# Kernel optimization log

Measured on AMD Instinct MI355X. Metric: run time of the kernel, lower is better.

Reference implementation:

```python
import jax, jax.numpy as jnp
import numpy as np

N, E, IN_CH, C, H, L, NCLS = 4096, 131072, 512, 256, 4, 3, 2
DH = C // H  # MHA head dim


def _ln(x, g, b, eps=1e-5):
    mu = x.mean(-1, keepdims=True)
    var = ((x - mu) ** 2).mean(-1, keepdims=True)
    return (x - mu) * jax.lax.rsqrt(var + eps) * g + b


def _gelu(x):
    return jax.nn.gelu(x, approximate=False)  # torch nn.GELU default (erf)


def _gatv2(x, src, dst, wl, wr, att, b):
    # x: [N,C]; wl/wr: [H*C, C]; att: [H,C]; b: [C]
    xl = (x @ wl.T).reshape(N, H, C)  # source transform
    e = jax.nn.leaky_relu(xl[src] + (x @ wr.T).reshape(N, H, C)[dst], 0.2)  # [Et,H,C]
    score = jnp.einsum('ehc,hc->eh', e, att)  # [Et,H]
    m = jax.ops.segment_max(score, dst, num_segments=N)
    ex = jnp.exp(score - m[dst])
    denom = jax.ops.segment_sum(ex, dst, num_segments=N)
    alpha = ex / denom[dst]  # segment softmax over incoming edges
    out = jax.ops.segment_sum(alpha[:, :, None] * xl[src], dst, num_segments=N)
    return out.mean(axis=1) + b  # concat=False -> head mean


def _mha(x, in_w, in_b, out_w, out_b):
    qkv = x @ in_w.T + in_b  # [N,3C]
    q, k, v = [t.reshape(N, H, DH) for t in jnp.split(qkv, 3, axis=-1)]
    scores = jnp.einsum('nhd,mhd->hnm', q, k) / np.sqrt(DH)
    probs = jax.nn.softmax(scores, axis=-1)
    o = jnp.einsum('hnm,mhd->nhd', probs, v).reshape(N, C)
    return o @ out_w.T + out_b


def setup_inputs() -> dict:
    key = jax.random.key(0)
    ks = iter(jax.random.split(key, 64))
    s = lambda shape, sc=0.05: jax.random.normal(next(ks), shape, jnp.float32) * sc
    d = {
        'x': jax.random.normal(next(ks), (N, IN_CH), jnp.float32),
        'edge_index': jax.random.randint(next(ks), (2, E), 0, N, jnp.int32),
        'in_w': s((C, IN_CH)), 'in_b': jnp.zeros((C,), jnp.float32),
        'gat_wl': s((L, H * C, C)), 'gat_wr': s((L, H * C, C)),
        'gat_att': s((L, H, C)), 'gat_b': jnp.zeros((L, C), jnp.float32),
        'mha_in_w': s((L, 3 * C, C)), 'mha_in_b': jnp.zeros((L, 3 * C), jnp.float32),
        'mha_out_w': s((L, C, C)), 'mha_out_b': jnp.zeros((L, C), jnp.float32),
        'ln1_g': jnp.ones((L, C), jnp.float32), 'ln1_b': jnp.zeros((L, C), jnp.float32),
        'ln2_g': jnp.ones((L, C), jnp.float32), 'ln2_b': jnp.zeros((L, C), jnp.float32),
        'ln3_g': jnp.ones((L, C), jnp.float32), 'ln3_b': jnp.zeros((L, C), jnp.float32),
        'ffn_w1': s((L, 2 * C, C)), 'ffn_b1': jnp.zeros((L, 2 * C), jnp.float32),
        'ffn_w2': s((L, C, 2 * C)), 'ffn_b2': jnp.zeros((L, C), jnp.float32),
        'out_w1': s((C, C)), 'out_b1': jnp.zeros((C,), jnp.float32),
        'out_w2': s((NCLS, C)), 'out_b2': jnp.zeros((NCLS,), jnp.float32),
    }
    return d


def reference(x, edge_index, in_w, in_b, gat_wl, gat_wr, gat_att, gat_b,
              mha_in_w, mha_in_b, mha_out_w, mha_out_b,
              ln1_g, ln1_b, ln2_g, ln2_b, ln3_g, ln3_b,
              ffn_w1, ffn_b1, ffn_w2, ffn_b2,
              out_w1, out_b1, out_w2, out_b2):
    # add self loops (PyG GATv2Conv default)
    loop = jnp.arange(N, dtype=edge_index.dtype)
    src = jnp.concatenate([edge_index[0], loop])
    dst = jnp.concatenate([edge_index[1], loop])

    h = x @ in_w.T + in_b  # input_proj
    for l in range(L):
        local = _gatv2(h, src, dst, gat_wl[l], gat_wr[l], gat_att[l], gat_b[l])
        h = _ln(h + local, ln1_g[l], ln1_b[l])
        attn = _mha(h, mha_in_w[l], mha_in_b[l], mha_out_w[l], mha_out_b[l])
        h = _ln(h + attn, ln2_g[l], ln2_b[l])
        ffn = _gelu(h @ ffn_w1[l].T + ffn_b1[l]) @ ffn_w2[l].T + ffn_b2[l]
        h = _ln(h + ffn, ln3_g[l], ln3_b[l])
    h = _gelu(h @ out_w1.T + out_b1)
    return h @ out_w2.T + out_b2
```

## Files before the change

### kernel.cpp

```cpp
#include <hip/hip_runtime.h>
#include <cstdint>
#include <cstddef>

typedef unsigned short u16;
typedef __bf16 bf16x8 __attribute__((ext_vector_type(8)));
typedef float f32x4 __attribute__((ext_vector_type(4)));

constexpr int kN  = 4096;
constexpr int kE  = 131072;
constexpr int kET = kE + kN;
constexpr int kIn = 512;
constexpr int kC  = 256;
constexpr int kL  = 3;

constexpr int NSPLIT = 4;
constexpr int KSPAN  = kN / NSPLIT;
constexpr int NSTEP  = KSPAN / 64;

__device__ __forceinline__ u16 f2bf(float f) {
    unsigned u = __builtin_bit_cast(unsigned, f);
    u += 0x7fffu + ((u >> 16) & 1u);
    return (u16)(u >> 16);
}
__device__ __forceinline__ float bf2f(u16 s) {
    unsigned u = ((unsigned)s) << 16;
    return __builtin_bit_cast(float, u);
}
__device__ __forceinline__ float gelu_erf(float x) {
    return 0.5f * x * (1.f + erff(x * 0.70710678118654752f));
}
__device__ __forceinline__ void gload_lds16(const u16* gsrc, u16* ldst) {
    __builtin_amdgcn_global_load_lds(
        (const __attribute__((address_space(1))) unsigned int*)gsrc,
        (__attribute__((address_space(3))) unsigned int*)ldst, 16, 0, 0);
}
__device__ __forceinline__ float dpp_ror_add16(float x) {
    int t;
    t = __builtin_amdgcn_update_dpp(0, __builtin_bit_cast(int, x), 0x121, 0xf, 0xf, true);
    x += __builtin_bit_cast(float, t);
    t = __builtin_amdgcn_update_dpp(0, __builtin_bit_cast(int, x), 0x122, 0xf, 0xf, true);
    x += __builtin_bit_cast(float, t);
    t = __builtin_amdgcn_update_dpp(0, __builtin_bit_cast(int, x), 0x124, 0xf, 0xf, true);
    x += __builtin_bit_cast(float, t);
    t = __builtin_amdgcn_update_dpp(0, __builtin_bit_cast(int, x), 0x128, 0xf, 0xf, true);
    x += __builtin_bit_cast(float, t);
    return x;
}
__device__ __forceinline__ void unpack8(uint4 u, float* x) {
    x[0] = __builtin_bit_cast(float, u.x << 16);
    x[1] = __builtin_bit_cast(float, u.x & 0xffff0000u);
    x[2] = __builtin_bit_cast(float, u.y << 16);
    x[3] = __builtin_bit_cast(float, u.y & 0xffff0000u);
    x[4] = __builtin_bit_cast(float, u.z << 16);
    x[5] = __builtin_bit_cast(float, u.z & 0xffff0000u);
    x[6] = __builtin_bit_cast(float, u.w << 16);
    x[7] = __builtin_bit_cast(float, u.w & 0xffff0000u);
}

__global__ void cast_all(
    const float* __restrict__ x, const float* __restrict__ in_w,
    const float* __restrict__ gwl, const float* __restrict__ gwr,
    const float* __restrict__ minw, const float* __restrict__ moutw,
    const float* __restrict__ f1, const float* __restrict__ f2,
    const float* __restrict__ o1,
    u16* __restrict__ xbf, u16* __restrict__ wbf) {
    int i = blockIdx.x * 256 + threadIdx.x;
    if (i >= 1359872) return;
    const float* s;
    u16* dbase;
    int sj, dj;
    if (i < 524288) {
        s = x; dbase = xbf; sj = i; dj = i;
    } else if (i < 557056) {
        s = in_w; dbase = wbf; sj = i - 524288; dj = sj;
    } else if (i < 753664) {
        int j = i - 557056; int l = j >> 16, wi = j & 65535;
        s = gwl; dbase = wbf; sj = j; dj = 32768 + l * 131072 + wi;
    } else if (i < 950272) {
        int j = i - 753664; int l = j >> 16, wi = j & 65535;
        s = gwr; dbase = wbf; sj = j; dj = 32768 + l * 131072 + 65536 + wi;
    } else if (i < 1097728) {
        s = minw; dbase = wbf; sj = i - 950272; dj = 425984 + sj;
    } else if (i < 1146880) {
        s = moutw; dbase = wbf; sj = i - 1097728; dj = 573440 + sj;
    } else if (i < 1245184) {
        s = f1; dbase = wbf; sj = i - 1146880; dj = 622592 + sj;
    } else if (i < 1343488) {
        s = f2; dbase = wbf; sj = i - 1245184; dj = 720896 + sj;
    } else {
        s = o1; dbase = wbf; sj = i - 1343488; dj = 819200 + sj;
    }
    float4 v = ((const float4*)s)[sj];
    ushort4 o;
    o.x = f2bf(v.x); o.y = f2bf(v.y); o.z = f2bf(v.z); o.w = f2bf(v.w);
    ((ushort4*)dbase)[dj] = o;
}

__global__ void csr_count(const int* __restrict__ ei, int* __restrict__ cnt) {
    int e = blockIdx.x * 256 + threadIdx.x;
    if (e >= kET) return;
    int d = (e < kE) ? ei[kE + e] : (e - kE);
    atomicAdd(cnt + d, 1);
}

__global__ __launch_bounds__(1024) void csr_scan(int* __restrict__ cnt_cur, int* __restrict__ off) {
    __shared__ int lds[1024];
    int t = threadIdx.x;
    int c[4], s = 0;
#pragma unroll
    for (int j = 0; j < 4; ++j) { c[j] = cnt_cur[t * 4 + j]; s += c[j]; }
    lds[t] = s;
    __syncthreads();
    for (int d = 1; d < 1024; d <<= 1) {
        int v = (t >= d) ? lds[t - d] : 0;
        __syncthreads();
        lds[t] += v;
        __syncthreads();
    }
    int excl = lds[t] - s;
#pragma unroll
    for (int j = 0; j < 4; ++j) { off[t * 4 + j] = excl; cnt_cur[t * 4 + j] = excl; excl += c[j]; }
    if (t == 1023) off[4096] = excl;
}

__global__ void csr_scatter(const int* __restrict__ ei, int* __restrict__ cur, int* __restrict__ csrc) {
    int e = blockIdx.x * 256 + threadIdx.x;
    if (e >= kET) return;
    int s, d;
    if (e < kE) { s = ei[e]; d = ei[kE + e]; } else { s = d = e - kE; }
    int pos = atomicAdd(cur + d, 1);
    csrc[pos] = s;
}

template <int BM, int K, int ACT, int WF32, int WBF16>
__global__ __launch_bounds__(256) void gemm_st(
    const u16* __restrict__ A, const u16* __restrict__ W,
    const float* __restrict__ bias, float* __restrict__ Cf,
    u16* __restrict__ Cb, int N) {
    constexpr int BK = 32;
    constexpr int NK = K / BK;
    constexpr int MF = BM / 32;
    int tid = threadIdx.x;
    int w = tid >> 6, lane = tid & 63;
    int wr = w >> 1, wc = w & 1;
    int g = lane >> 4, r = lane & 15;
    int bm = blockIdx.y * BM;
    int bn = blockIdx.x * 64;
    __shared__ __align__(16) u16 Ab[2][BM * BK];
    __shared__ __align__(16) u16 Bb[2][64 * BK];
    int srow = w * 16 + (lane >> 2);
    int scol = (lane & 3) * 8;
    auto stage = [&](int buf, int k0) {
#pragma unroll
        for (int i = 0; i < BM / 64; ++i)
            gload_lds16(A + (size_t)(bm + i * 64 + srow) * K + k0 + scol,
                        &Ab[buf][(i * 64 + w * 16) * BK]);
        gload_lds16(W + (size_t)(bn + srow) * K + k0 + scol, &Bb[buf][w * 16 * BK]);
    };
    f32x4 acc[MF][2] = {};
    stage(0, 0);
    __syncthreads();
    for (int st = 0; st < NK; ++st) {
        int cur = st & 1;
        if (st + 1 < NK) stage(cur ^ 1, (st + 1) * BK);
        const u16* Al = &Ab[cur][0];
        const u16* Bl = &Bb[cur][0];
        bf16x8 bf[2];
#pragma unroll
        for (int u = 0; u < 2; ++u)
            bf[u] = *(const bf16x8*)(Bl + (wc * 32 + u * 16 + r) * BK + g * 8);
#pragma unroll
        for (int t = 0; t < MF; ++t) {
            bf16x8 af = *(const bf16x8*)(Al + (wr * (BM / 2) + t * 16 + r) * BK + g * 8);
#pragma unroll
            for (int u = 0; u < 2; ++u)
                acc[t][u] = __builtin_amdgcn_mfma_f32_16x16x32_bf16(af, bf[u], acc[t][u], 0, 0, 0);
        }
        __syncthreads();
    }
    int r0 = bm + wr * (BM / 2) + g * 4;
    int c0 = bn + wc * 32 + r;
#pragma unroll
    for (int t = 0; t < MF; ++t)
#pragma unroll
        for (int u = 0; u < 2; ++u)
#pragma unroll
            for (int e = 0; e < 4; ++e) {
                int row = r0 + t * 16 + e, col = c0 + u * 16;
                float v = acc[t][u][e];
                if (bias) v += bias[col];
                if (ACT == 1) v = gelu_erf(v);
                if (WF32) Cf[(size_t)row * N + col] = v;
                if (WBF16) Cb[(size_t)row * N + col] = f2bf(v);
            }
}

__global__ __launch_bounds__(256) void gemm_qkv(
    const u16* __restrict__ A, const u16* __restrict__ W,
    const float* __restrict__ bias,
    u16* __restrict__ Qb, u16* __restrict__ Kb, u16* __restrict__ VTb) {
    constexpr int BK = 32, K = 256, NK = 8, BM = 128, MF = 4;
    int tid = threadIdx.x;
    int w = tid >> 6, lane = tid & 63;
    int wr = w >> 1, wc = w & 1;
    int g = lane >> 4, r = lane & 15;
    int bm = blockIdx.y * BM;
    int bn = blockIdx.x * 64;
    __shared__ __align__(16) u16 Ab[2][BM * BK];
    __shared__ __align__(16) u16 Bb[2][64 * BK];
    int srow = w * 16 + (lane >> 2);
    int scol = (lane & 3) * 8;
    auto stage = [&](int buf, int k0) {
#pragma unroll
        for (int i = 0; i < 2; ++i)
            gload_lds16(A + (size_t)(bm + i * 64 + srow) * K + k0 + scol,
                        &Ab[buf][(i * 64 + w * 16) * BK]);
        gload_lds16(W + (size_t)(bn + srow) * K + k0 + scol, &Bb[buf][w * 16 * BK]);
    };
    f32x4 acc[MF][2] = {};
    stage(0, 0);
    __syncthreads();
    for (int st = 0; st < NK; ++st) {
        int cur = st & 1;
        if (st + 1 < NK) stage(cur ^ 1, (st + 1) * BK);
        const u16* Al = &Ab[cur][0];
        const u16* Bl = &Bb[cur][0];
        bf16x8 bf[2];
#pragma unroll
        for (int u = 0; u < 2; ++u)
            bf[u] = *(const bf16x8*)(Bl + (wc * 32 + u * 16 + r) * BK + g * 8);
#pragma unroll
        for (int t = 0; t < MF; ++t) {
            bf16x8 af = *(const bf16x8*)(Al + (wr * 64 + t * 16 + r) * BK + g * 8);
#pragma unroll
            for (int u = 0; u < 2; ++u)
                acc[t][u] = __builtin_amdgcn_mfma_f32_16x16x32_bf16(af, bf[u], acc[t][u], 0, 0, 0);
        }
        __syncthreads();
    }
    constexpr float QS = 0.125f * 1.4426950408889634f;
    int region = blockIdx.x >> 2;
    int head = blockIdx.x & 3;
    int r0 = bm + wr * 64 + g * 4;
    if (region == 2) {
#pragma unroll
        for (int t = 0; t < MF; ++t)
#pragma unroll
            for (int u = 0; u < 2; ++u) {
                int d = wc * 32 + u * 16 + r;
                int col = bn + d;
                ushort4 vo;
                vo.x = f2bf(acc[t][u][0] + bias[col]);
                vo.y = f2bf(acc[t][u][1] + bias[col]);
                vo.z = f2bf(acc[t][u][2] + bias[col]);
                vo.w = f2bf(acc[t][u][3] + bias[col]);
                *(ushort4*)(VTb + ((size_t)head * 64 + d) * kN + r0 + t * 16) = vo;
            }
    } else {
        u16* dst = (region == 0) ? Qb : Kb;
        float sc = (region == 0) ? QS : 1.f;
#pragma unroll
        for (int t = 0; t < MF; ++t)
#pragma unroll
            for (int u = 0; u < 2; ++u)
#pragma unroll
                for (int e = 0; e < 4; ++e) {
                    int d = wc * 32 + u * 16 + r;
                    int row = r0 + t * 16 + e;
                    dst[((size_t)head * kN + row) * 64 + d] =
                        f2bf((acc[t][u][e] + bias[bn + d]) * sc);
                }
    }
}

template <int K>
__global__ __launch_bounds__(256) void gemm_128(
    const u16* __restrict__ A, const u16* __restrict__ W,
    u16* __restrict__ Cb, int N) {
    constexpr int BK = 32;
    constexpr int NK = K / BK;
    int tid = threadIdx.x;
    int w = tid >> 6, lane = tid & 63;
    int wr = w >> 1, wc = w & 1;
    int g = lane >> 4, r = lane & 15;
    int bm = blockIdx.y * 128;
    int bn = blockIdx.x * 128;
    __shared__ __align__(16) u16 Ab[2][128 * BK];
    __shared__ __align__(16) u16 Bb[2][128 * BK];
    int srd = lane >> 2;
    int schunk = ((lane & 3) ^ ((lane >> 3) & 3)) * 8;
    auto stage = [&](int buf, int k0) {
#pragma unroll
        for (int i = 0; i < 2; ++i) {
            int rowA = bm + i * 64 + w * 16 + srd;
            int rowB = bn + i * 64 + w * 16 + srd;
            gload_lds16(A + (size_t)rowA * K + k0 + schunk, &Ab[buf][(i * 64 + w * 16) * BK]);
            gload_lds16(W + (size_t)rowB * K + k0 + schunk, &Bb[buf][(i * 64 + w * 16) * BK]);
        }
    };
    f32x4 acc[4][4] = {};
    stage(0, 0);
    __syncthreads();
    int rs = (r >> 1) & 3;
    for (int st = 0; st < NK; ++st) {
        int cur = st & 1;
        if (st + 1 < NK) stage(cur ^ 1, (st + 1) * BK);
        const u16* Al = &Ab[cur][0];
        const u16* Bl = &Bb[cur][0];
        bf16x8 bf[4];
#pragma unroll
        for (int u = 0; u < 4; ++u)
            bf[u] = *(const bf16x8*)(Bl + (wc * 64 + u * 16 + r) * BK + ((g ^ rs) * 8));
#pragma unroll
        for (int t = 0; t < 4; ++t) {
            bf16x8 af = *(const bf16x8*)(Al + (wr * 64 + t * 16 + r) * BK + ((g ^ rs) * 8));
#pragma unroll
            for (int u = 0; u < 4; ++u)
                acc[t][u] = __builtin_amdgcn_mfma_f32_16x16x32_bf16(af, bf[u], acc[t][u], 0, 0, 0);
        }
        __syncthreads();
    }
#pragma unroll
    for (int t = 0; t < 4; ++t)
#pragma unroll
        for (int u = 0; u < 4; ++u)
#pragma unroll
            for (int e = 0; e < 4; ++e) {
                int row = bm + wr * 64 + t * 16 + g * 4 + e;
                int col = bn + wc * 64 + u * 16 + r;
                Cb[(size_t)row * N + col] = f2bf(acc[t][u][e]);
            }
}

template <int BM, int K>
__global__ __launch_bounds__(256) void gemm_ln(
    const u16* __restrict__ A, const u16* __restrict__ W,
    const float* __restrict__ bias,
    const float* __restrict__ lng, const float* __restrict__ lnb,
    float* __restrict__ h, u16* __restrict__ hbf) {
    constexpr int BK = 32;
    constexpr int NK = K / BK;
    constexpr int MT = BM / 16;
    int tid = threadIdx.x;
    int w = tid >> 6, lane = tid & 63;
    int g = lane >> 4, r = lane & 15;
    int bm = blockIdx.x * BM;
    __shared__ __align__(16) u16 Ab[2][BM * BK];
    __shared__ __align__(16) u16 Bb[2][256 * BK];
    __shared__ float sums[BM][4][2];
    int srd = lane >> 2;
    int schunk = ((lane & 3) ^ ((lane >> 3) & 3)) * 8;
    auto stage = [&](int buf, int k0) {
        if (w < MT)
            gload_lds16(A + (size_t)(bm + w * 16 + srd) * K + k0 + schunk,
                        &Ab[buf][(w * 16) * BK]);
#pragma unroll
        for (int i = 0; i < 4; ++i)
            gload_lds16(W + (size_t)(w * 64 + i * 16 + srd) * K + k0 + schunk,
                        &Bb[buf][(w * 64 + i * 16) * BK]);
    };
    f32x4 acc[MT][4] = {};
    stage(0, 0);
    __syncthreads();
    int rs = (r >> 1) & 3;
    for (int st = 0; st < NK; ++st) {
        int cur = st & 1;
        if (st + 1 < NK) stage(cur ^ 1, (st + 1) * BK);
        const u16* Al = &Ab[cur][0];
        const u16* Bl = &Bb[cur][0];
        bf16x8 bf[4];
#pragma unroll
        for (int u = 0; u < 4; ++u)
            bf[u] = *(const bf16x8*)(Bl + (w * 64 + u * 16 + r) * BK + ((g ^ rs) * 8));
#pragma unroll
        for (int t = 0; t < MT; ++t) {
            bf16x8 af = *(const bf16x8*)(Al + (t * 16 + r) * BK + ((g ^ rs) * 8));
#pragma unroll
            for (int u = 0; u < 4; ++u)
                acc[t][u] = __builtin_amdgcn_mfma_f32_16x16x32_bf16(af, bf[u], acc[t][u], 0, 0, 0);
        }
        __syncthreads();
    }
    float val[MT][4][4];
#pragma unroll
    for (int t = 0; t < MT; ++t)
#pragma unroll
        for (int e = 0; e < 4; ++e) {
            int row = bm + t * 16 + g * 4 + e;
            float s1 = 0.f, s2 = 0.f;
#pragma unroll
            for (int u = 0; u < 4; ++u) {
                int col = w * 64 + u * 16 + r;
                float v = acc[t][u][e] + bias[col] + h[(size_t)row * kC + col];
                val[t][u][e] = v;
                s1 += v;
                s2 += v * v;
            }
            s1 = dpp_ror_add16(s1);
            s2 = dpp_ror_add16(s2);
            if (r == 0) {
                sums[t * 16 + g * 4 + e][w][0] = s1;
                sums[t * 16 + g * 4 + e][w][1] = s2;
            }
        }
    __syncthreads();
#pragma unroll
    for (int t = 0; t < MT; ++t)
#pragma unroll
        for (int e = 0; e < 4; ++e) {
            int lr = t * 16 + g * 4 + e;
            int row = bm + lr;
            float S1 = sums[lr][0][0] + sums[lr][1][0] + sums[lr][2][0] + sums[lr][3][0];
            float S2 = sums[lr][0][1] + sums[lr][1][1] + sums[lr][2][1] + sums[lr][3][1];
            float mu = S1 * (1.f / kC);
            float rstd = rsqrtf(S2 * (1.f / kC) - mu * mu + 1e-5f);
#pragma unroll
            for (int u = 0; u < 4; ++u) {
                int col = w * 64 + u * 16 + r;
                float y = (val[t][u][e] - mu) * rstd * lng[col] + lnb[col];
                h[(size_t)row * kC + col] = y;
                hbf[(size_t)row * kC + col] = f2bf(y);
            }
        }
}

__global__ __launch_bounds__(256) void gat_agg(
    const u16* __restrict__ xg,
    const float* __restrict__ att, const float* __restrict__ gb,
    const int* __restrict__ off, const int* __restrict__ srcs,
    const float* __restrict__ lng, const float* __restrict__ lnb,
    float* __restrict__ h, u16* __restrict__ hbf) {
    int n = blockIdx.x;
    int w = threadIdx.x >> 6, lane = threadIdx.x & 63;
    int q = lane >> 4, t = lane & 15;
    int cb = w * 256 + t * 16;

    uint4 xru0 = *(const uint4*)(xg + (size_t)n * 2048 + 1024 + cb);
    uint4 xru1 = *(const uint4*)(xg + (size_t)n * 2048 + 1024 + cb + 8);
    float xrv[16];
    unpack8(xru0, xrv); unpack8(xru1, xrv + 8);
    float att6[16], att4[16];
#pragma unroll
    for (int j = 0; j < 16; j += 4) {
        float4 a4 = *(const float4*)(att + cb + j);
        att6[j] = 0.6f * a4.x; att6[j + 1] = 0.6f * a4.y;
        att6[j + 2] = 0.6f * a4.z; att6[j + 3] = 0.6f * a4.w;
        att4[j] = (2.f / 3.f) * att6[j]; att4[j + 1] = (2.f / 3.f) * att6[j + 1];
        att4[j + 2] = (2.f / 3.f) * att6[j + 2]; att4[j + 3] = (2.f / 3.f) * att6[j + 3];
    }

    int i0 = off[n], i1 = off[n + 1];
    float m = -1e30f, ls = 0.f;
    float acc[16] = {};
    int i = i0 + q;
    uint4 p0a, p1a, p0b, p1b;
    if (i < i1) {
        int s = srcs[i];
        p0a = *(const uint4*)(xg + (size_t)s * 2048 + cb);
        p1a = *(const uint4*)(xg + (size_t)s * 2048 + cb + 8);
    }
    if (i + 4 < i1) {
        int s = srcs[i + 4];
        p0b = *(const uint4*)(xg + (size_t)s * 2048 + cb);
        p1b = *(const uint4*)(xg + (size_t)s * 2048 + cb + 8);
    }
    while (i < i1) {
        uint4 c0 = p0a, c1 = p1a;
        p0a = p0b; p1a = p1b;
        if (i + 8 < i1) {
            int s2 = srcs[i + 8];
            p0b = *(const uint4*)(xg + (size_t)s2 * 2048 + cb);
            p1b = *(const uint4*)(xg + (size_t)s2 * 2048 + cb + 8);
        }
        float x[16];
        unpack8(c0, x); unpack8(c1, x + 8);
        float p = 0.f;
#pragma unroll
        for (int j = 0; j < 16; ++j) {
            float e = x[j] + xrv[j];
            p = fmaf(att6[j], e, p);
            p = fmaf(att4[j], __builtin_fabsf(e), p);
        }
        p = dpp_ror_add16(p);
        if (p > m) {
            float c = __expf(m - p);
            ls = ls * c + 1.f;
#pragma unroll
            for (int j = 0; j < 16; ++j) acc[j] = acc[j] * c + x[j];
            m = p;
        } else {
            float pw = __expf(p - m);
            ls += pw;
#pragma unroll
            for (int j = 0; j < 16; ++j) acc[j] = fmaf(pw, x[j], acc[j]);
        }
        i += 4;
    }
    float mm = fmaxf(m, __shfl_xor(m, 16));
    mm = fmaxf(mm, __shfl_xor(mm, 32));
    float c = __expf(m - mm);
    ls *= c;
    ls += __shfl_xor(ls, 16);
    ls += __shfl_xor(ls, 32);
#pragma unroll
    for (int j = 0; j < 16; ++j) {
        float a = acc[j] * c;
        a += __shfl_xor(a, 16);
        a += __shfl_xor(a, 32);
        acc[j] = a;
    }
    float inv = 1.f / ls;
    __shared__ float red[4][256];
    __shared__ float rs[8];
    if (q == 0) {
#pragma unroll
        for (int j = 0; j < 16; ++j) red[w][t * 16 + j] = acc[j] * inv;
    }
    __syncthreads();
    int cc = threadIdx.x;
    float vsum = 0.25f * (red[0][cc] + red[1][cc] + red[2][cc] + red[3][cc]) + gb[cc];
    float v = h[(size_t)n * kC + cc] + vsum;
    float s1 = v, s2 = v * v;
    for (int d = 1; d < 64; d <<= 1) { s1 += __shfl_xor(s1, d); s2 += __shfl_xor(s2, d); }
    if (lane == 0) { rs[w] = s1; rs[4 + w] = s2; }
    __syncthreads();
    s1 = rs[0] + rs[1] + rs[2] + rs[3];
    s2 = rs[4] + rs[5] + rs[6] + rs[7];
    float mu = s1 * (1.f / kC);
    float rstd = rsqrtf(s2 * (1.f / kC) - mu * mu + 1e-5f);
    float y = (v - mu) * rstd * lng[cc] + lnb[cc];
    h[(size_t)n * kC + cc] = y;
    hbf[(size_t)n * kC + cc] = f2bf(y);
}

__global__ __launch_bounds__(256, 2) void mha_mfma3(
    const u16* __restrict__ Qb, const u16* __restrict__ Kb,
    const u16* __restrict__ VTb, float* __restrict__ opart, float* __restrict__ mlpart) {
    int qt = blockIdx.x, head = blockIdx.y, sp = blockIdx.z;
    int tid = threadIdx.x;
    int w = tid >> 6, lane = tid & 63;
    int g = lane >> 4, r = lane & 15;
    int q0 = qt * 128;
    const u16* QhA = Qb + ((size_t)head * kN + q0 + w * 16) * 64;
    const u16* QhB = QhA + (size_t)64 * 64;
    const u16* Kh = Kb + (size_t)head * kN * 64;
    const u16* VTh = VTb + (size_t)head * 64 * kN;
    __shared__ u16 Kt[2][64 * 64];
    __shared__ u16 Vt[2][64 * 64];
    __shared__ u16 plds[4][2][16 * 64];
    int srow = w * 8 + (lane >> 3);
    int schunk = ((lane & 7) ^ ((lane >> 3) & 7)) * 8;
    int kbase = sp * KSPAN;

    bf16x8 qfA0 = *(const bf16x8*)(QhA + r * 64 + g * 8);
    bf16x8 qfA1 = *(const bf16x8*)(QhA + r * 64 + 32 + g * 8);
    bf16x8 qfB0 = *(const bf16x8*)(QhB + r * 64 + g * 8);
    bf16x8 qfB1 = *(const bf16x8*)(QhB + r * 64 + 32 + g * 8);

    auto stage = [&](int buf, int k0) {
#pragma unroll
        for (int i = 0; i < 2; ++i) {
            int row = i * 32 + srow;
            gload_lds16(Kh + (size_t)(k0 + row) * 64 + schunk, &Kt[buf][(i * 32 + w * 8) * 64]);
            gload_lds16(VTh + (size_t)row * kN + k0 + schunk, &Vt[buf][(i * 32 + w * 8) * 64]);
        }
    };

    f32x4 oA[4] = {}, oB[4] = {};
    float mA = -3.0e38f, lA = 0.f, mB = -3.0e38f, lB = 0.f;

    stage(0, kbase);
    __syncthreads();

    int rx = r & 7;
    for (int st = 0; st < NSTEP; ++st) {
        int cur = st & 1;
        if (st + 1 < NSTEP) stage(cur ^ 1, kbase + (st + 1) * 64);
        const u16* Kl = &Kt[cur][0];
        const u16* Vl = &Vt[cur][0];
        {
            f32x4 stt[4] = {};
#pragma unroll
            for (int t = 0; t < 4; ++t) {
                bf16x8 kf0 = *(const bf16x8*)(Kl + (16 * t + r) * 64 + ((0 + g) ^ rx) * 8);
                bf16x8 kf1 = *(const bf16x8*)(Kl + (16 * t + r) * 64 + ((4 + g) ^ rx) * 8);
                stt[t] = __builtin_amdgcn_mfma_f32_16x16x32_bf16(kf0, qfA0, stt[t], 0, 0, 0);
                stt[t] = __builtin_amdgcn_mfma_f32_16x16x32_bf16(kf1, qfA1, stt[t], 0, 0, 0);
            }
            float pm = stt[0][0];
#pragma unroll
            for (int t = 0; t < 4; ++t)
#pragma unroll
                for (int e = 0; e < 4; ++e) pm = fmaxf(pm, stt[t][e]);
            pm = fmaxf(pm, __shfl_xor(pm, 16));
            pm = fmaxf(pm, __shfl_xor(pm, 32));
            if (__any(pm > mA)) {
                float mn = fmaxf(mA, pm);
                float corr = __builtin_amdgcn_exp2f(mA - mn);
                lA *= corr;
                float corrq[4];
#pragma unroll
                for (int e = 0; e < 4; ++e) corrq[e] = __shfl(corr, g * 4 + e);
#pragma unroll
                for (int dt = 0; dt < 4; ++dt)
#pragma unroll
                    for (int e = 0; e < 4; ++e) oA[dt][e] *= corrq[e];
                mA = mn;
            }
            float lsx = 0.f;
#pragma unroll
            for (int t = 0; t < 4; ++t) {
                ushort4 pk;
                float p0 = __builtin_amdgcn_exp2f(stt[t][0] - mA);
                float p1 = __builtin_amdgcn_exp2f(stt[t][1] - mA);
                float p2 = __builtin_amdgcn_exp2f(stt[t][2] - mA);
                float p3 = __builtin_amdgcn_exp2f(stt[t][3] - mA);
                lsx += (p0 + p1) + (p2 + p3);
                pk.x = f2bf(p0); pk.y = f2bf(p1); pk.z = f2bf(p2); pk.w = f2bf(p3);
                int lc = (2 * t + (g >> 1)) ^ rx;
                *(ushort4*)(&plds[w][0][r * 64 + lc * 8 + (g & 1) * 4]) = pk;
            }
            lsx += __shfl_xor(lsx, 16);
            lsx += __shfl_xor(lsx, 32);
            lA += lsx;
        }
        {
            f32x4 stt[4] = {};
#pragma unroll
            for (int t = 0; t < 4; ++t) {
                bf16x8 kf0 = *(const bf16x8*)(Kl + (16 * t + r) * 64 + ((0 + g) ^ rx) * 8);
                bf16x8 kf1 = *(const bf16x8*)(Kl + (16 * t + r) * 64 + ((4 + g) ^ rx) * 8);
                stt[t] = __builtin_amdgcn_mfma_f32_16x16x32_bf16(kf0, qfB0, stt[t], 0, 0, 0);
                stt[t] = __builtin_amdgcn_mfma_f32_16x16x32_bf16(kf1, qfB1, stt[t], 0, 0, 0);
            }
            float pm = stt[0][0];
#pragma unroll
            for (int t = 0; t < 4; ++t)
#pragma unroll
                for (int e = 0; e < 4; ++e) pm = fmaxf(pm, stt[t][e]);
            pm = fmaxf(pm, __shfl_xor(pm, 16));
            pm = fmaxf(pm, __shfl_xor(pm, 32));
            if (__any(pm > mB)) {
                float mn = fmaxf(mB, pm);
                float corr = __builtin_amdgcn_exp2f(mB - mn);
                lB *= corr;
                float corrq[4];
#pragma unroll
                for (int e = 0; e < 4; ++e) corrq[e] = __shfl(corr, g * 4 + e);
#pragma unroll
                for (int dt = 0; dt < 4; ++dt)
#pragma unroll
                    for (int e = 0; e < 4; ++e) oB[dt][e] *= corrq[e];
                mB = mn;
            }
            float lsx = 0.f;
#pragma unroll
            for (int t = 0; t < 4; ++t) {
                ushort4 pk;
                float p0 = __builtin_amdgcn_exp2f(stt[t][0] - mB);
                float p1 = __builtin_amdgcn_exp2f(stt[t][1] - mB);
                float p2 = __builtin_amdgcn_exp2f(stt[t][2] - mB);
                float p3 = __builtin_amdgcn_exp2f(stt[t][3] - mB);
                lsx += (p0 + p1) + (p2 + p3);
                pk.x = f2bf(p0); pk.y = f2bf(p1); pk.z = f2bf(p2); pk.w = f2bf(p3);
                int lc = (2 * t + (g >> 1)) ^ rx;
                *(ushort4*)(&plds[w][1][r * 64 + lc * 8 + (g & 1) * 4]) = pk;
            }
            lsx += __shfl_xor(lsx, 16);
            lsx += __shfl_xor(lsx, 32);
            lB += lsx;
        }
        bf16x8 paA0 = *(const bf16x8*)(&plds[w][0][r * 64 + (g ^ rx) * 8]);
        bf16x8 paA1 = *(const bf16x8*)(&plds[w][0][r * 64 + ((4 + g) ^ rx) * 8]);
        bf16x8 paB0 = *(const bf16x8*)(&plds[w][1][r * 64 + (g ^ rx) * 8]);
        bf16x8 paB1 = *(const bf16x8*)(&plds[w][1][r * 64 + ((4 + g) ^ rx) * 8]);
#pragma unroll
        for (int dt = 0; dt < 4; ++dt) {
            bf16x8 vf0 = *(const bf16x8*)(Vl + (dt * 16 + r) * 64 + ((0 + g) ^ rx) * 8);
            bf16x8 vf1 = *(const bf16x8*)(Vl + (dt * 16 + r) * 64 + ((4 + g) ^ rx) * 8);
            oA[dt] = __builtin_amdgcn_mfma_f32_16x16x32_bf16(paA0, vf0, oA[dt], 0, 0, 0);
            oA[dt] = __builtin_amdgcn_mfma_f32_16x16x32_bf16(paA1, vf1, oA[dt], 0, 0, 0);
            oB[dt] = __builtin_amdgcn_mfma_f32_16x16x32_bf16(paB0, vf0, oB[dt], 0, 0, 0);
            oB[dt] = __builtin_amdgcn_mfma_f32_16x16x32_bf16(paB1, vf1, oB[dt], 0, 0, 0);
        }
        __syncthreads();
    }

    size_t slot = (size_t)(head * 32 + qt) * NSPLIT + sp;
    float* ob = opart + slot * 8192;
#pragma unroll
    for (int dt = 0; dt < 4; ++dt)
#pragma unroll
        for (int e = 0; e < 4; ++e) {
            ob[(w * 16 + g * 4 + e) * 64 + dt * 16 + r] = oA[dt][e];
            ob[(64 + w * 16 + g * 4 + e) * 64 + dt * 16 + r] = oB[dt][e];
        }
    float* mlb = mlpart + slot * 256;
    if (g == 0) {
        mlb[w * 16 + r] = mA;
        mlb[64 + w * 16 + r] = mB;
        mlb[128 + w * 16 + r] = lA;
        mlb[192 + w * 16 + r] = lB;
    }
}

__global__ __launch_bounds__(256) void mha_merge(
    const float* __restrict__ opart, const float* __restrict__ mlpart,
    u16* __restrict__ attnb) {
    int head = blockIdx.y;
    int q = blockIdx.x * 4 + (threadIdx.x >> 6);
    int d = threadIdx.x & 63;
    int qt = q >> 7, ql = q & 127;
    size_t sb = (size_t)(head * 32 + qt) * NSPLIT;
    float ms[NSPLIT], lsv[NSPLIT];
    float mstar = -3.0e38f;
#pragma unroll
    for (int s = 0; s < NSPLIT; ++s) {
        ms[s] = mlpart[(sb + s) * 256 + ql];
        lsv[s] = mlpart[(sb + s) * 256 + 128 + ql];
        mstar = fmaxf(mstar, ms[s]);
    }
    float acc = 0.f, lsum = 0.f;
#pragma unroll
    for (int s = 0; s < NSPLIT; ++s) {
        float wgt = __builtin_amdgcn_exp2f(ms[s] - mstar);
        lsum += lsv[s] * wgt;
        acc += opart[(sb + s) * 8192 + ql * 64 + d] * wgt;
    }
    attnb[(size_t)q * kC + head * 64 + d] = f2bf(acc / lsum);
}

__global__ __launch_bounds__(256) void final_out(
    const u16* __restrict__ tbf, const float* __restrict__ w2,
    const float* __restrict__ b2, float* __restrict__ out) {
    int row = blockIdx.x * 4 + (threadIdx.x >> 6);
    int lane = threadIdx.x & 63;
    const ushort4 tv = *(const ushort4*)(tbf + (size_t)row * 256 + lane * 4);
    float t0 = bf2f(tv.x), t1 = bf2f(tv.y), t2 = bf2f(tv.z), t3 = bf2f(tv.w);
    const float4 w0 = *(const float4*)(w2 + lane * 4);
    const float4 w1 = *(const float4*)(w2 + 256 + lane * 4);
    float d0 = t0 * w0.x + t1 * w0.y + t2 * w0.z + t3 * w0.w;
    float d1 = t0 * w1.x + t1 * w1.y + t2 * w1.z + t3 * w1.w;
    for (int d = 1; d < 64; d <<= 1) { d0 += __shfl_xor(d0, d); d1 += __shfl_xor(d1, d); }
    if (lane == 0) {
        out[(size_t)row * 2 + 0] = d0 + b2[0];
        out[(size_t)row * 2 + 1] = d1 + b2[1];
    }
}

extern "C" void kernel_launch(void* const* d_in, const int* in_sizes, int n_in,
                              void* d_out, int out_size, void* d_ws, size_t ws_size,
                              hipStream_t stream) {
    (void)in_sizes; (void)n_in; (void)out_size;
    const float* x        = (const float*)d_in[0];
    const int*   ei       = (const int*)d_in[1];
    const float* in_w     = (const float*)d_in[2];
    const float* in_b     = (const float*)d_in[3];
    const float* gat_wl   = (const float*)d_in[4];
    const float* gat_wr   = (const float*)d_in[5];
    const float* gat_att  = (const float*)d_in[6];
    const float* gat_b    = (const float*)d_in[7];
    const float* mha_in_w = (const float*)d_in[8];
    const float* mha_in_b = (const float*)d_in[9];
    const float* mha_out_w= (const float*)d_in[10];
    const float* mha_out_b= (const float*)d_in[11];
    const float* ln1_g = (const float*)d_in[12];
    const float* ln1_b = (const float*)d_in[13];
    const float* ln2_g = (const float*)d_in[14];
    const float* ln2_b = (const float*)d_in[15];
    const float* ln3_g = (const float*)d_in[16];
    const float* ln3_b = (const float*)d_in[17];
    const float* ffn_w1 = (const float*)d_in[18];
    const float* ffn_b1 = (const float*)d_in[19];
    const float* ffn_w2 = (const float*)d_in[20];
    const float* ffn_b2 = (const float*)d_in[21];
    const float* out_w1 = (const float*)d_in[22];
    const float* out_b1 = (const float*)d_in[23];
    const float* out_w2 = (const float*)d_in[24];
    const float* out_b2 = (const float*)d_in[25];
    float* out = (float*)d_out;

    char* ws = (char*)d_ws;
    size_t off = 0;
    auto alloc = [&](size_t bytes) -> void* {
        void* p = (void*)(ws + off);
        off += (bytes + 255) & ~(size_t)255;
        return p;
    };
    float* h     = (float*)alloc((size_t)kN * kC * 4);
    u16*   hbf   = (u16*)  alloc((size_t)kN * kC * 2);
    float* xlb   = (float*)alloc((size_t)kN * 1024 * 4);
    float* xrb   = (float*)alloc((size_t)kN * 1024 * 4);
    float* locb  = (float*)alloc((size_t)kN * kC * 4);
    u16*   attnb = (u16*)  alloc((size_t)kN * kC * 2);
    u16*   midb  = (u16*)  alloc((size_t)kN * 512 * 2);
    u16*   tbf   = (u16*)  alloc((size_t)kN * kC * 2);
    u16*   xbf   = (u16*)  alloc((size_t)kN * kIn * 2);
    u16*   wbf   = (u16*)  alloc((size_t)3342336 * 2);
    int*   coff  = (int*)  alloc((size_t)4097 * 4);
    int*   ccur  = (int*)  alloc((size_t)4096 * 4);
    int*   csrc  = (int*)  alloc((size_t)kET * 4);
    if (ws_size < off) return;

    u16* xgbf = (u16*)xlb;
    u16* Qb  = (u16*)xlb;
    u16* Kb  = Qb + (size_t)4 * kN * 64;
    u16* VTb = Kb + (size_t)4 * kN * 64;
    float* opart  = xrb;
    float* mlpart = locb;

    const size_t OFF_INW  = 0;
    const size_t OFF_GAT  = 131072;
    const size_t OFF_MIN  = 1703936;
    const size_t OFF_MOUT = 2293760;
    const size_t OFF_F1   = 2490368;
    const size_t OFF_F2   = 2883584;
    const size_t OFF_O1   = 3276800;

    cast_all<<<dim3((1359872 + 255) / 256), dim3(256), 0, stream>>>(
        x, in_w, gat_wl, gat_wr, mha_in_w, mha_out_w, ffn_w1, ffn_w2, out_w1,
        xbf, wbf);

    hipMemsetAsync(ccur, 0, 4096 * 4, stream);
    csr_count<<<dim3((kET + 255) / 256), dim3(256), 0, stream>>>(ei, ccur);
    csr_scan<<<dim3(1), dim3(1024), 0, stream>>>(ccur, coff);
    csr_scatter<<<dim3((kET + 255) / 256), dim3(256), 0, stream>>>(ei, ccur, csrc);

    gemm_st<64, 512, 0, 1, 1><<<dim3(kC / 64, kN / 64), dim3(256), 0, stream>>>(
        xbf, wbf + OFF_INW, in_b, h, hbf, kC);

    for (int l = 0; l < kL; ++l) {
        gemm_128<256><<<dim3(2048 / 128, kN / 128), dim3(256), 0, stream>>>(
            hbf, wbf + OFF_GAT + (size_t)l * 524288, xgbf, 2048);
        gat_agg<<<dim3(kN), dim3(256), 0, stream>>>(
            xgbf, gat_att + (size_t)l * 1024, gat_b + (size_t)l * kC, coff, csrc,
            ln1_g + (size_t)l * kC, ln1_b + (size_t)l * kC, h, hbf);

        gemm_qkv<<<dim3(768 / 64, kN / 128), dim3(256), 0, stream>>>(
            hbf, wbf + OFF_MIN + (size_t)l * 768 * kC, mha_in_b + (size_t)l * 768,
            Qb, Kb, VTb);
        mha_mfma3<<<dim3(kN / 128, 4, NSPLIT), dim3(256), 0, stream>>>(Qb, Kb, VTb, opart, mlpart);
        mha_merge<<<dim3(kN / 4, 4), dim3(256), 0, stream>>>(opart, mlpart, attnb);
        gemm_ln<16, 256><<<dim3(kN / 16), dim3(256), 0, stream>>>(
            attnb, wbf + OFF_MOUT + (size_t)l * kC * kC, mha_out_b + (size_t)l * kC,
            ln2_g + (size_t)l * kC, ln2_b + (size_t)l * kC, h, hbf);

        gemm_st<64, 256, 1, 0, 1><<<dim3(512 / 64, kN / 64), dim3(256), 0, stream>>>(
            hbf, wbf + OFF_F1 + (size_t)l * 512 * kC, ffn_b1 + (size_t)l * 512, nullptr, midb, 512);
        gemm_ln<16, 512><<<dim3(kN / 16), dim3(256), 0, stream>>>(
            midb, wbf + OFF_F2 + (size_t)l * kC * 512, ffn_b2 + (size_t)l * kC,
            ln3_g + (size_t)l * kC, ln3_b + (size_t)l * kC, h, hbf);
    }

    gemm_st<64, 256, 1, 0, 1><<<dim3(kC / 64, kN / 64), dim3(256), 0, stream>>>(
        hbf, wbf + OFF_O1, out_b1, nullptr, tbf, kC);
    final_out<<<dim3(kN / 4), dim3(256), 0, stream>>>(tbf, out_w2, out_b2, out);
}
```

Baseline: 477.2 us.

## Fuse FFN up-projection, GELU, down-projection and LayerNorm into one kernel

Replaces the separate FFN first GEMM (writing the 512-wide intermediate to global memory) and the second GEMM+LN kernel with a single kernel. Each 16-row block keeps the GELU output in LDS with a swizzled layout and streams both weight matrices through LDS, double-buffering W2. Separately, the CSR edge-count pass is folded into the weight-cast kernel to remove one launch. The fused kernel reloads the full W1 and W2 for every 16-row block, which raises weight traffic, and launches only 256 blocks.

```diff
diff --git a/kernel.cpp b/kernel.cpp
--- a/kernel.cpp
+++ b/kernel.cpp
@@ -63,9 +63,16 @@
     const float* __restrict__ minw, const float* __restrict__ moutw,
     const float* __restrict__ f1, const float* __restrict__ f2,
     const float* __restrict__ o1,
-    u16* __restrict__ xbf, u16* __restrict__ wbf) {
+    u16* __restrict__ xbf, u16* __restrict__ wbf,
+    const int* __restrict__ ei, int* __restrict__ cnt) {
     int i = blockIdx.x * 256 + threadIdx.x;
-    if (i >= 1359872) return;
+    if (i >= 1495040) return;
+    if (i >= 1359872) {
+        int e = i - 1359872;
+        int d = (e < kE) ? ei[kE + e] : (e - kE);
+        atomicAdd(cnt + d, 1);
+        return;
+    }
     const float* s;
     u16* dbase;
     int sj, dj;
@@ -96,13 +103,6 @@
     ((ushort4*)dbase)[dj] = o;
 }
 
-__global__ void csr_count(const int* __restrict__ ei, int* __restrict__ cnt) {
-    int e = blockIdx.x * 256 + threadIdx.x;
-    if (e >= kET) return;
-    int d = (e < kE) ? ei[kE + e] : (e - kE);
-    atomicAdd(cnt + d, 1);
-}
-
 __global__ __launch_bounds__(1024) void csr_scan(int* __restrict__ cnt_cur, int* __restrict__ off) {
     __shared__ int lds[1024];
     int t = threadIdx.x;
@@ -422,6 +422,109 @@
                 hbf[(size_t)row * kC + col] = f2bf(y);
             }
         }
+}
+
+__global__ __launch_bounds__(256) void ffn_fused(
+    const u16* __restrict__ Ah, const u16* __restrict__ W1,
+    const float* __restrict__ b1, const u16* __restrict__ W2,
+    const float* __restrict__ b2,
+    const float* __restrict__ lng, const float* __restrict__ lnb,
+    float* __restrict__ h, u16* __restrict__ hbf) {
+    int tid = threadIdx.x;
+    int w = tid >> 6, lane = tid & 63;
+    int g = lane >> 4, r = lane & 15;
+    int bm = blockIdx.x * 16;
+    __shared__ __align__(16) u16 WS[512 * 32];
+    __shared__ __align__(16) u16 midl[16 * 512];
+    __shared__ float sums[16][4][2];
+    int srow = lane >> 2;
+    int scol = (lane & 3) * 8;
+    int rx = r & 7;
+    f32x4 acc1[8] = {};
+    for (int st = 0; st < 8; ++st) {
+        int k0 = st * 32;
+        __syncthreads();
+#pragma unroll
+        for (int i = 0; i < 8; ++i)
+            gload_lds16(W1 + (size_t)(w * 128 + i * 16 + srow) * 256 + k0 + scol,
+                        &WS[(w * 128 + i * 16) * 32]);
+        __syncthreads();
+        bf16x8 bA = *(const bf16x8*)(Ah + (size_t)(bm + r) * 256 + k0 + g * 8);
+#pragma unroll
+        for (int u = 0; u < 8; ++u) {
+            bf16x8 af = *(const bf16x8*)(&WS[(w * 128 + u * 16 + r) * 32 + g * 8]);
+            acc1[u] = __builtin_amdgcn_mfma_f32_16x16x32_bf16(af, bA, acc1[u], 0, 0, 0);
+        }
+    }
+    __syncthreads();
+#pragma unroll
+    for (int u = 0; u < 8; ++u) {
+        int cb = w * 128 + u * 16 + g * 4;
+        int c16 = cb >> 3;
+        int half = (cb >> 2) & 1;
+        ushort4 mo;
+        mo.x = f2bf(gelu_erf(acc1[u][0] + b1[cb + 0]));
+        mo.y = f2bf(gelu_erf(acc1[u][1] + b1[cb + 1]));
+        mo.z = f2bf(gelu_erf(acc1[u][2] + b1[cb + 2]));
+        mo.w = f2bf(gelu_erf(acc1[u][3] + b1[cb + 3]));
+        *(ushort4*)(&midl[r * 512 + (c16 ^ rx) * 8 + half * 4]) = mo;
+    }
+#pragma unroll
+    for (int i = 0; i < 4; ++i)
+        gload_lds16(W2 + (size_t)(w * 64 + i * 16 + srow) * 512 + scol,
+                    &WS[(w * 64 + i * 16) * 32]);
+    __syncthreads();
+    f32x4 acc2[4] = {};
+    for (int st = 0; st < 16; ++st) {
+        int cur = st & 1;
+        if (st + 1 < 16) {
+            int k0n = (st + 1) * 32;
+#pragma unroll
+            for (int i = 0; i < 4; ++i)
+                gload_lds16(W2 + (size_t)(w * 64 + i * 16 + srow) * 512 + k0n + scol,
+                            &WS[((cur ^ 1) * 256 + w * 64 + i * 16) * 32]);
+        }
+        int cA = st * 4 + g;
+        bf16x8 afm = *(const bf16x8*)(&midl[r * 512 + (cA ^ rx) * 8]);
+#pragma unroll
+        for (int u = 0; u < 4; ++u) {
+            bf16x8 bf = *(const bf16x8*)(&WS[(cur * 256 + w * 64 + u * 16 + r) * 32 + g * 8]);
+            acc2[u] = __builtin_amdgcn_mfma_f32_16x16x32_bf16(afm, bf, acc2[u], 0, 0, 0);
+        }
+        __syncthreads();
+    }
+    float val[4][4];
+#pragma unroll
+    for (int e = 0; e < 4; ++e) {
+        int row = bm + g * 4 + e;
+        float s1 = 0.f, s2 = 0.f;
+#pragma unroll
+        for (int u = 0; u < 4; ++u) {
+            int col = w * 64 + u * 16 + r;
+            float v = acc2[u][e] + b2[col] + h[(size_t)row * kC + col];
+            val[u][e] = v;
+            s1 += v; s2 += v * v;
+        }
+        s1 = dpp_ror_add16(s1);
+        s2 = dpp_ror_add16(s2);
+        if (r == 0) { sums[g * 4 + e][w][0] = s1; sums[g * 4 + e][w][1] = s2; }
+    }
+    __syncthreads();
+#pragma unroll
+    for (int e = 0; e < 4; ++e) {
+        int lr = g * 4 + e, row = bm + lr;
+        float S1 = sums[lr][0][0] + sums[lr][1][0] + sums[lr][2][0] + sums[lr][3][0];
+        float S2 = sums[lr][0][1] + sums[lr][1][1] + sums[lr][2][1] + sums[lr][3][1];
+        float mu = S1 * (1.f / kC);
+        float rstd = rsqrtf(S2 * (1.f / kC) - mu * mu + 1e-5f);
+#pragma unroll
+        for (int u = 0; u < 4; ++u) {
+            int col = w * 64 + u * 16 + r;
+            float y = (val[u][e] - mu) * rstd * lng[col] + lnb[col];
+            h[(size_t)row * kC + col] = y;
+            hbf[(size_t)row * kC + col] = f2bf(y);
+        }
+    }
 }
 
 __global__ __launch_bounds__(256) void gat_agg(
@@ -793,7 +896,6 @@
     float* xrb   = (float*)alloc((size_t)kN * 1024 * 4);
     float* locb  = (float*)alloc((size_t)kN * kC * 4);
     u16*   attnb = (u16*)  alloc((size_t)kN * kC * 2);
-    u16*   midb  = (u16*)  alloc((size_t)kN * 512 * 2);
     u16*   tbf   = (u16*)  alloc((size_t)kN * kC * 2);
     u16*   xbf   = (u16*)  alloc((size_t)kN * kIn * 2);
     u16*   wbf   = (u16*)  alloc((size_t)3342336 * 2);
@@ -817,12 +919,10 @@
     const size_t OFF_F2   = 2883584;
     const size_t OFF_O1   = 3276800;
 
-    cast_all<<<dim3((1359872 + 255) / 256), dim3(256), 0, stream>>>(
+    hipMemsetAsync(ccur, 0, 4096 * 4, stream);
+    cast_all<<<dim3(1495040 / 256), dim3(256), 0, stream>>>(
         x, in_w, gat_wl, gat_wr, mha_in_w, mha_out_w, ffn_w1, ffn_w2, out_w1,
-        xbf, wbf);
-
-    hipMemsetAsync(ccur, 0, 4096 * 4, stream);
-    csr_count<<<dim3((kET + 255) / 256), dim3(256), 0, stream>>>(ei, ccur);
+        xbf, wbf, ei, ccur);
     csr_scan<<<dim3(1), dim3(1024), 0, stream>>>(ccur, coff);
     csr_scatter<<<dim3((kET + 255) / 256), dim3(256), 0, stream>>>(ei, ccur, csrc);
 
@@ -845,10 +945,9 @@
             attnb, wbf + OFF_MOUT + (size_t)l * kC * kC, mha_out_b + (size_t)l * kC,
             ln2_g + (size_t)l * kC, ln2_b + (size_t)l * kC, h, hbf);
 
-        gemm_st<64, 256, 1, 0, 1><<<dim3(512 / 64, kN / 64), dim3(256), 0, stream>>>(
-            hbf, wbf + OFF_F1 + (size_t)l * 512 * kC, ffn_b1 + (size_t)l * 512, nullptr, midb, 512);
-        gemm_ln<16, 512><<<dim3(kN / 16), dim3(256), 0, stream>>>(
-            midb, wbf + OFF_F2 + (size_t)l * kC * 512, ffn_b2 + (size_t)l * kC,
+        ffn_fused<<<dim3(kN / 16), dim3(256), 0, stream>>>(
+            hbf, wbf + OFF_F1 + (size_t)l * 512 * kC, ffn_b1 + (size_t)l * 512,
+            wbf + OFF_F2 + (size_t)l * kC * 512, ffn_b2 + (size_t)l * kC,
             ln3_g + (size_t)l * kC, ln3_b + (size_t)l * kC, h, hbf);
     }
 
```

Result: slower. 489.7 us (+2.6%).
